# Kernel tuning notes

Measured on AMD Instinct MI355X. Metric: run time of the kernel, lower is better.

Reference implementation:

```python
import jax, jax.numpy as jnp
import numpy as np

B, T, D, H, K, V = 2, 2048, 2048, 16, 128, 128


def _l2norm(x, eps=1e-12):
    # F.normalize(p=2, dim=-1)
    n = jnp.sqrt(jnp.sum(x * x, axis=-1, keepdims=True))
    return x / jnp.maximum(n, eps)


def setup_inputs() -> dict:
    key = jax.random.key(0)
    ks = jax.random.split(key, 7)
    s = D ** -0.5
    return {
        "x": jax.random.normal(ks[0], (B, T, D), jnp.float32),
        "Wq": jax.random.normal(ks[1], (H * K, D), jnp.float32) * s,
        "Wk": jax.random.normal(ks[2], (H * K, D), jnp.float32) * s,
        "Wv": jax.random.normal(ks[3], (H * V, D), jnp.float32) * s,
        "Wa": jax.random.normal(ks[4], (H, D), jnp.float32) * s,
        "ba": jnp.zeros((H,), jnp.float32),
        "Wb": jax.random.normal(ks[5], (H, D), jnp.float32) * s,
        "bb": jnp.zeros((H,), jnp.float32),
    }


def _forward(x, Wq, Wk, Wv, Wa, ba, Wb, bb):
    Bq, Tq, _ = x.shape
    # projections (nn.Linear: y = x @ W.T)
    q = _l2norm(jnp.einsum('btd,od->bto', x, Wq).reshape(Bq, Tq, H, K))
    k = _l2norm(jnp.einsum('btd,od->bto', x, Wk).reshape(Bq, Tq, H, K))
    v = jnp.einsum('btd,od->bto', x, Wv).reshape(Bq, Tq, H, V)
    alpha = jax.nn.sigmoid(jnp.einsum('btd,hd->bth', x, Wa) + ba)          # [B,T,H] decay in (0,1)
    beta = jax.nn.softplus(jnp.einsum('btd,hd->bth', x, Wb) + bb) * K ** (-0.5)

    # gated delta rule recurrence over time (vectorized over B,H):
    #   S_t = a_t * S_{t-1} (I - b_t k_t k_t^T) + b_t v_t k_t^T ;  o_t = S_t q_t
    def step(S, inp):
        q_t, k_t, v_t, a_t, b_t = inp  # [B,H,K],[B,H,K],[B,H,V],[B,H],[B,H]
        Sd = S * a_t[..., None, None]                              # decay  [B,H,V,K]
        pred = jnp.einsum('bhvk,bhk->bhv', Sd, k_t)                # S k
        u = b_t[..., None] * (v_t - pred)                          # delta update [B,H,V]
        S_new = Sd + u[..., None] * k_t[:, :, None, :]             # rank-1 write
        o_t = jnp.einsum('bhvk,bhk->bhv', S_new, q_t)
        return S_new, o_t

    S0 = jnp.zeros((Bq, H, V, K), x.dtype)
    xs = (q.transpose(1, 0, 2, 3), k.transpose(1, 0, 2, 3),
          v.transpose(1, 0, 2, 3), alpha.transpose(1, 0, 2), beta.transpose(1, 0, 2))
    _, o = jax.lax.scan(step, S0, xs)
    return o.transpose(1, 0, 2, 3)  # [B,T,H,V]


def reference(x, Wq, Wk, Wv, Wa, ba, Wb, bb):
    return _forward(x, Wq, Wk, Wv, Wa, ba, Wb, bb)
```

## Files before the change

kernel.cpp:

```cpp
#include <hip/hip_runtime.h>
#include <math.h>

#define BB 2
#define TT 2048
#define DD 2048
#define HH 16
#define KK 128

typedef _Float16 h4 __attribute__((ext_vector_type(4)));
typedef _Float16 v8h __attribute__((ext_vector_type(8)));
typedef float v4f __attribute__((ext_vector_type(4)));
typedef float f2 __attribute__((ext_vector_type(2)));
typedef unsigned int u2v __attribute__((ext_vector_type(2)));

__global__ __launch_bounds__(256) void gemm_nt3(const float* __restrict__ A,
                                                const float* __restrict__ W0,
                                                const float* __restrict__ W1,
                                                const float* __restrict__ W2,
                                                float* __restrict__ Cbase,
                                                int M, int N, int Kd) {
  __shared__ float As[8][128];
  __shared__ float Bs[8][128];
  const int z = blockIdx.z;
  const float* W = (z == 0) ? W0 : (z == 1) ? W1 : W2;
  float* C = Cbase + (size_t)z * M * N;
  const int tid = threadIdx.x;
  const int bm = blockIdx.y * 128;
  const int bn = blockIdx.x * 128;
  const int lrow = tid >> 1;
  const int lcol = (tid & 1) * 4;
  const int rm = (tid >> 4) * 8;
  const int rn = (tid & 15) * 8;
  const float* Ap = A + (size_t)(bm + lrow) * Kd + lcol;
  const float* Wp = W + (size_t)(bn + lrow) * Kd + lcol;
  float acc[8][8];
#pragma unroll
  for (int i = 0; i < 8; i++)
#pragma unroll
    for (int j = 0; j < 8; j++) acc[i][j] = 0.f;
  float4 av = *(const float4*)Ap;
  float4 wv = *(const float4*)Wp;
  for (int d0 = 0; d0 < Kd; d0 += 8) {
    __syncthreads();
    As[lcol + 0][lrow] = av.x; As[lcol + 1][lrow] = av.y;
    As[lcol + 2][lrow] = av.z; As[lcol + 3][lrow] = av.w;
    Bs[lcol + 0][lrow] = wv.x; Bs[lcol + 1][lrow] = wv.y;
    Bs[lcol + 2][lrow] = wv.z; Bs[lcol + 3][lrow] = wv.w;
    __syncthreads();
    if (d0 + 8 < Kd) {
      av = *(const float4*)(Ap + d0 + 8);
      wv = *(const float4*)(Wp + d0 + 8);
    }
#pragma unroll
    for (int kk = 0; kk < 8; kk++) {
      const float4 a0 = *(const float4*)&As[kk][rm];
      const float4 a1 = *(const float4*)&As[kk][rm + 4];
      const float4 b0 = *(const float4*)&Bs[kk][rn];
      const float4 b1 = *(const float4*)&Bs[kk][rn + 4];
      const float ar[8] = {a0.x, a0.y, a0.z, a0.w, a1.x, a1.y, a1.z, a1.w};
      const float br[8] = {b0.x, b0.y, b0.z, b0.w, b1.x, b1.y, b1.z, b1.w};
#pragma unroll
      for (int i = 0; i < 8; i++)
#pragma unroll
        for (int j = 0; j < 8; j++) acc[i][j] = fmaf(ar[i], br[j], acc[i][j]);
    }
  }
#pragma unroll
  for (int i = 0; i < 8; i++) {
    float* cp = C + (size_t)(bm + rm + i) * N + bn + rn;
    float4 c0 = {acc[i][0], acc[i][1], acc[i][2], acc[i][3]};
    float4 c1 = {acc[i][4], acc[i][5], acc[i][6], acc[i][7]};
    *(float4*)cp = c0;
    *(float4*)(cp + 4) = c1;
  }
}

__global__ __launch_bounds__(256) void convert_f16(
    const float* __restrict__ x, const float* __restrict__ Wq,
    const float* __restrict__ Wk, const float* __restrict__ Wv,
    _Float16* __restrict__ xh, _Float16* __restrict__ Wf) {
  const size_t N4X = (size_t)BB * TT * DD / 4;
  const size_t N4W = (size_t)(HH * KK) * DD / 4;
  const size_t i = (size_t)blockIdx.x * 256 + threadIdx.x;
  if (i < N4X) {
    const float4 v = ((const float4*)x)[i];
    h4 hi;
    hi.x = (_Float16)v.x; hi.y = (_Float16)v.y;
    hi.z = (_Float16)v.z; hi.w = (_Float16)v.w;
    ((h4*)xh)[i] = hi;
  } else {
    const size_t j = i - N4X;
    const float* Ws = (j < N4W) ? Wq : (j < 2 * N4W) ? Wk : Wv;
    const size_t jj = (j < N4W) ? j : (j < 2 * N4W) ? (j - N4W) : (j - 2 * N4W);
    const float4 v = ((const float4*)Ws)[jj];
    h4 hi;
    hi.x = (_Float16)v.x; hi.y = (_Float16)v.y;
    hi.z = (_Float16)v.z; hi.w = (_Float16)v.w;
    ((h4*)Wf)[j] = hi;
  }
}

#define GLDS(gp, lp)                                              \
  __builtin_amdgcn_global_load_lds(                               \
      (const __attribute__((address_space(1))) void*)(gp),        \
      (__attribute__((address_space(3))) void*)(lp), 16, 0, 0)

__global__ __launch_bounds__(256) void gemm_mfma(
    const _Float16* __restrict__ xh, const _Float16* __restrict__ Wf,
    float* __restrict__ Cbase) {
  __shared__ float4 lraw[1024];
  _Float16* Ah = (_Float16*)lraw;
  _Float16* Bs = Ah + 4096;

  const int z = blockIdx.z;
  const _Float16* W = Wf + (size_t)z * DD * (HH * KK);
  float* C = Cbase + (size_t)z * (BB * TT) * (HH * KK);

  const int tid = threadIdx.x;
  const int w = tid >> 6;
  const int lane = tid & 63;
  const int bm = blockIdx.y * 128;
  const int bn = blockIdx.x * 128;
  const int wm = (w & 1) * 64;
  const int wn = (w >> 1) * 64;
  const int m16 = lane & 15;
  const int quad = lane >> 4;

  const _Float16* gA = xh + (size_t)(bm + (tid >> 2)) * DD + (tid & 3) * 8;
  const _Float16* gB = W + (size_t)(bn + (tid >> 2)) * DD + (tid & 3) * 8;
  const int lb = w * 512;

  v4f acc[4][4];
#pragma unroll
  for (int i = 0; i < 4; i++)
#pragma unroll
    for (int j = 0; j < 4; j++) acc[i][j] = (v4f){0.f, 0.f, 0.f, 0.f};

  for (int d0 = 0; d0 < DD; d0 += 32) {
    GLDS(gA + d0, Ah + lb);
    GLDS(gA + d0 + 64 * DD, Ah + 2048 + lb);
    GLDS(gB + d0, Bs + lb);
    GLDS(gB + d0 + 64 * DD, Bs + 2048 + lb);
    __syncthreads();
    v8h ah[4], bw[4];
#pragma unroll
    for (int i = 0; i < 4; i++) {
      ah[i] = *(const v8h*)&Ah[(wm + i * 16 + m16) * 32 + quad * 8];
      bw[i] = *(const v8h*)&Bs[(wn + i * 16 + m16) * 32 + quad * 8];
    }
#pragma unroll
    for (int mi = 0; mi < 4; mi++)
#pragma unroll
      for (int ni = 0; ni < 4; ni++)
        acc[mi][ni] = __builtin_amdgcn_mfma_f32_16x16x32_f16(ah[mi], bw[ni],
                                                             acc[mi][ni], 0, 0, 0);
    __syncthreads();
  }
#pragma unroll
  for (int mi = 0; mi < 4; mi++) {
#pragma unroll
    for (int r = 0; r < 4; r++) {
      float* cp =
          C + (size_t)(bm + wm + mi * 16 + quad * 4 + r) * (HH * KK) + bn + wn + m16;
#pragma unroll
      for (int ni = 0; ni < 4; ni++) cp[ni * 16] = acc[mi][ni][r];
    }
  }
}

__global__ __launch_bounds__(64) void ab_proj(const float* __restrict__ x,
                                              const float* __restrict__ Wa,
                                              const float* __restrict__ ba,
                                              const float* __restrict__ Wb,
                                              const float* __restrict__ bb,
                                              float* __restrict__ abq) {
  const int row = blockIdx.x;
  const int g = blockIdx.y;
  const int h0 = (g & 1) * 8;
  const bool isA = (g < 2);
  const float* W = isA ? Wa : Wb;
  const int lane = threadIdx.x;
  const float* xr = x + (size_t)row * DD;
  float acc[8];
#pragma unroll
  for (int j = 0; j < 8; j++) acc[j] = 0.f;
  for (int d = lane; d < DD; d += 64) {
    const float xv = xr[d];
#pragma unroll
    for (int j = 0; j < 8; j++)
      acc[j] = fmaf(xv, W[(size_t)(h0 + j) * DD + d], acc[j]);
  }
#pragma unroll
  for (int j = 0; j < 8; j++) {
#pragma unroll
    for (int off = 32; off > 0; off >>= 1) acc[j] += __shfl_xor(acc[j], off, 64);
  }
  if (lane == 0) {
    if (isA) {
#pragma unroll
      for (int j = 0; j < 8; j++) {
        const float z = acc[j] + ba[h0 + j];
        abq[((size_t)row * HH + h0 + j) * 4 + 0] = 1.0f / (1.0f + expf(-z));
      }
    } else {
#pragma unroll
      for (int j = 0; j < 8; j++) {
        const float z = acc[j] + bb[h0 + j];
        const float sp = (z > 20.f) ? z : log1pf(expf(z));
        abq[((size_t)row * HH + h0 + j) * 4 + 1] = sp * 0.08838834764831845f;
      }
    }
  }
}

__global__ __launch_bounds__(256) void norm_qk(float* __restrict__ q,
                                               float* __restrict__ k,
                                               float* __restrict__ abq) {
  const int vec = blockIdx.x * 4 + (threadIdx.x >> 6);
  const int l = threadIdx.x & 63;
  float* qp = q + (size_t)vec * 128;
  float* kp = k + (size_t)vec * 128;
  float q0 = qp[l], q1 = qp[l + 64];
  float k0 = kp[l], k1 = kp[l + 64];
  float sq = q0 * q0 + q1 * q1;
  float sk = k0 * k0 + k1 * k1;
#pragma unroll
  for (int off = 32; off > 0; off >>= 1) {
    sq += __shfl_xor(sq, off, 64);
    sk += __shfl_xor(sk, off, 64);
  }
  const float iq = 1.0f / fmaxf(sqrtf(sq), 1e-12f);
  const float ik = 1.0f / fmaxf(sqrtf(sk), 1e-12f);
  q0 *= iq; q1 *= iq; k0 *= ik; k1 *= ik;
  qp[l] = q0; qp[l + 64] = q1;
  kp[l] = k0; kp[l + 64] = k1;
  float pq = q0 * k0 + q1 * k1;
#pragma unroll
  for (int off = 32; off > 0; off >>= 1) pq += __shfl_xor(pq, off, 64);
  if (l == 0) abq[(size_t)vec * 4 + 2] = pq;
}

#define DPP_ADD(x, ctrl)                                                     \
  ((x) + __int_as_float(__builtin_amdgcn_update_dpp(                         \
             0, __float_as_int(x), (ctrl), 0xF, 0xF, true)))

__device__ __forceinline__ float xadd32(float x) {
  const u2v r = __builtin_amdgcn_permlane32_swap(__float_as_uint(x),
                                                 __float_as_uint(x), false,
                                                 false);
  return __uint_as_float(r.x) + __uint_as_float(r.y);
}

#define SCAN_STEP(kc, qc, vc, ac, jj)                                          \
  {                                                                            \
    const f2 ka = {kc.x, kc.y};                                                \
    const f2 kb2 = {kc.z, kc.w};                                               \
    const f2 qa = {qc.x, qc.y};                                                \
    const f2 qb2 = {qc.z, qc.w};                                               \
    const f2 pdk = __builtin_elementwise_fma(Sb, kb2, Sa * ka);                \
    const f2 pdq = __builtin_elementwise_fma(Sb, qb2, Sa * qa);                \
    float dk = pdk.x + pdk.y;                                                  \
    float dq = pdq.x + pdq.y;                                                  \
    dk = DPP_ADD(dk, 0xB1);  dq = DPP_ADD(dq, 0xB1);             \
    dk = DPP_ADD(dk, 0x4E);  dq = DPP_ADD(dq, 0x4E);             \
    dk = DPP_ADD(dk, 0x141); dq = DPP_ADD(dq, 0x141);            \
    dk = DPP_ADD(dk, 0x140); dq = DPP_ADD(dq, 0x140);            \
    dk = xadd32(dk);         dq = xadd32(dq);                    \
    const float u = ac.y * fmaf(-ac.x, dk, vc);                                \
    const float oo = fmaf(ac.x, dq, u * ac.z);                                 \
    const f2 a2 = {ac.x, ac.x};                                                \
    const f2 u2 = {u, u};                                                      \
    Sa = __builtin_elementwise_fma(a2, Sa, u2 * ka);                           \
    Sb = __builtin_elementwise_fma(a2, Sb, u2 * kb2);                          \
    obuf = (ks == (jj)) ? oo : obuf;                                           \
  }

#define PD 8

__global__ __launch_bounds__(256, 2) void scan_kernel(
    const float* __restrict__ q, const float* __restrict__ k,
    const float* __restrict__ v, const float* __restrict__ abq,
    float* __restrict__ o) {
  const int bid = blockIdx.x;
  const int bh = bid & 31;
  const int s = bid >> 5;
  const int h = bh & 15;
  const int b = bh >> 4;
  const int tid = threadIdx.x;
  const int w = tid >> 6;
  const int lane = tid & 63;
  const int rg = (lane >> 4) & 1;
  const int ks = (lane & 15) | ((lane >> 5) << 4);
  const int vrow = s * 8 + w * 2 + rg;

  const size_t base = (size_t)b * TT * 2048 + (size_t)h * KK;
  const float* kU = k + base;
  const float* qU = q + base;
  const float* vU = v + base;
  const float* aU = abq + ((size_t)b * TT * HH + h) * 4;
  float* oU = o + base;
  const int vks = ks * 4;

  f2 Sa = {0.f, 0.f}, Sb = {0.f, 0.f};
  float obuf = 0.f;

  float4 kf[PD], qf[PD], af[PD];
  float vf[PD];
#pragma unroll
  for (int d = 0; d < PD; d++) {
    kf[d] = *(const float4*)(kU + vks + d * 2048);
    qf[d] = *(const float4*)(qU + vks + d * 2048);
    vf[d] = vU[vrow + d * 2048];
    af[d] = *(const float4*)(aU + d * 64);
  }

  int off = 0;
  int aoff = 0;
  for (int t0 = 0; t0 < TT - PD; t0 += PD) {
#pragma unroll
    for (int j = 0; j < PD; j++) {
      SCAN_STEP(kf[j], qf[j], vf[j], af[j], j);
      kf[j] = *(const float4*)(kU + vks + off + (j + PD) * 2048);
      qf[j] = *(const float4*)(qU + vks + off + (j + PD) * 2048);
      vf[j] = vU[vrow + off + (j + PD) * 2048];
      af[j] = *(const float4*)(aU + aoff + (j + PD) * 64);
      __builtin_amdgcn_sched_barrier(0);
    }
    if (ks < 8) oU[vrow + off + ks * 2048] = obuf;
    off += PD * 2048;
    aoff += PD * 64;
  }
#pragma unroll
  for (int j = 0; j < PD; j++) {
    SCAN_STEP(kf[j], qf[j], vf[j], af[j], j);
  }
  if (ks < 8) oU[vrow + off + ks * 2048] = obuf;
}

extern "C" void kernel_launch(void* const* d_in, const int* in_sizes, int n_in,
                              void* d_out, int out_size, void* d_ws,
                              size_t ws_size, hipStream_t stream) {
  const float* x = (const float*)d_in[0];
  const float* Wq = (const float*)d_in[1];
  const float* Wk = (const float*)d_in[2];
  const float* Wv = (const float*)d_in[3];
  const float* Wa = (const float*)d_in[4];
  const float* ba = (const float*)d_in[5];
  const float* Wb = (const float*)d_in[6];
  const float* bb = (const float*)d_in[7];
  float* out = (float*)d_out;
  float* ws = (float*)d_ws;

  const size_t PROJ = (size_t)BB * TT * HH * KK;
  const size_t NABQ = (size_t)BB * TT * HH * 4;
  float* qw = ws;
  float* kw = ws + PROJ;
  float* vw = ws + 2 * PROJ;
  float* abq = ws + 3 * PROJ;
  _Float16* xh = (_Float16*)(abq + NABQ);
  _Float16* Wf = xh + (size_t)BB * TT * DD;
  const size_t NEED = (3 * PROJ + NABQ) * 4 +
                      ((size_t)BB * TT * DD + 3 * (size_t)(HH * KK) * DD) * 2;

  const int M = BB * TT;
  const int N = HH * KK;
  if (ws_size >= NEED) {
    const int cgrid = (int)(((size_t)BB * TT * DD / 4 + 3 * (size_t)N * DD / 4) / 256);
    convert_f16<<<cgrid, 256, 0, stream>>>(x, Wq, Wk, Wv, xh, Wf);
    gemm_mfma<<<dim3(N / 128, M / 128, 3), 256, 0, stream>>>(xh, Wf, qw);
  } else {
    gemm_nt3<<<dim3(N / 128, M / 128, 3), 256, 0, stream>>>(x, Wq, Wk, Wv, qw,
                                                            M, N, DD);
  }
  ab_proj<<<dim3(M, 4), 64, 0, stream>>>(x, Wa, ba, Wb, bb, abq);
  norm_qk<<<(BB * TT * HH) / 4, 256, 0, stream>>>(qw, kw, abq);
  scan_kernel<<<BB * HH * 16, 256, 0, stream>>>(qw, kw, vw, abq, out);
}
```

Baseline: 726.0 us.

## Double-buffer k/q/gate tiles in LDS via direct global-to-LDS loads in scan

The recurrent scan kernel no longer loads k, q and gate vectors into per-thread register prefetch arrays. Instead, each workgroup stages groups of 8 timesteps into double-buffered shared memory using direct global-to-LDS loads, with explicit vmcnt waits and workgroup barriers, and reads them back from LDS during compute. The goal is to cut redundant global traffic and register pressure from the per-lane prefetch pipeline. The cost is two block-wide barriers per 8-step group on a latency-bound serial recurrence, plus extra LDS reads on the critical path.

```diff
diff --git a/kernel.cpp b/kernel.cpp
--- a/kernel.cpp
+++ b/kernel.cpp
@@ -251,7 +251,10 @@
   return __uint_as_float(r.x) + __uint_as_float(r.y);
 }
 
-#define SCAN_STEP(kc, qc, vc, ac, jj)                                          \
+#define SBAR() asm volatile("s_barrier" ::: "memory")
+#define WAITV(n) asm volatile("s_waitcnt vmcnt(" #n ")" ::: "memory")
+
+#define SCAN_MATH(kc, qc, vc, ac, jj, obname)                                  \
   {                                                                            \
     const f2 ka = {kc.x, kc.y};                                                \
     const f2 kb2 = {kc.z, kc.w};                                               \
@@ -272,15 +275,40 @@
     const f2 u2 = {u, u};                                                      \
     Sa = __builtin_elementwise_fma(a2, Sa, u2 * ka);                           \
     Sb = __builtin_elementwise_fma(a2, Sb, u2 * kb2);                          \
-    obuf = (ks == (jj)) ? oo : obuf;                                           \
-  }
-
-#define PD 8
+    obname = (ks == (jj)) ? oo : obname;                                       \
+  }
+
+#define STAGE(bi, tg)                                                          \
+  {                                                                            \
+    const float* gk =                                                          \
+        kU + (size_t)((tg) + 2 * w + (lane >> 5)) * 2048 + (lane & 31) * 4;    \
+    GLDS(gk, &Kb[bi][2 * w][0]);                                               \
+    const float* gq =                                                          \
+        qU + (size_t)((tg) + 2 * w + (lane >> 5)) * 2048 + (lane & 31) * 4;    \
+    GLDS(gq, &Qb[bi][2 * w][0]);                                               \
+    if (lane < 8) GLDS(aU + (size_t)((tg) + lane) * 64, &Ab[bi][0][0]);        \
+    _Pragma("unroll") for (int jj = 0; jj < 8; jj++)                           \
+        vf##bi[jj] = vU[vrow + (size_t)((tg) + jj) * 2048];                    \
+  }
+
+#define COMPUTE_GROUP(bi, obname)                                              \
+  float obname = 0.f;                                                          \
+  _Pragma("unroll") for (int j = 0; j < 8; j++) {                              \
+    const float4 kc = *(const float4*)&Kb[bi][j][ks4];                         \
+    const float4 qc = *(const float4*)&Qb[bi][j][ks4];                         \
+    const float4 ac = *(const float4*)&Ab[bi][j][0];                           \
+    const float vc = vf##bi[j];                                                \
+    SCAN_MATH(kc, qc, vc, ac, j, obname);                                      \
+  }
 
 __global__ __launch_bounds__(256, 2) void scan_kernel(
     const float* __restrict__ q, const float* __restrict__ k,
     const float* __restrict__ v, const float* __restrict__ abq,
     float* __restrict__ o) {
+  __shared__ float Kb[2][8][128];
+  __shared__ float Qb[2][8][128];
+  __shared__ float Ab[2][8][4];
+
   const int bid = blockIdx.x;
   const int bh = bid & 31;
   const int s = bid >> 5;
@@ -291,6 +319,7 @@
   const int lane = tid & 63;
   const int rg = (lane >> 4) & 1;
   const int ks = (lane & 15) | ((lane >> 5) << 4);
+  const int ks4 = ks * 4;
   const int vrow = s * 8 + w * 2 + rg;
 
   const size_t base = (size_t)b * TT * 2048 + (size_t)h * KK;
@@ -299,42 +328,44 @@
   const float* vU = v + base;
   const float* aU = abq + ((size_t)b * TT * HH + h) * 4;
   float* oU = o + base;
-  const int vks = ks * 4;
 
   f2 Sa = {0.f, 0.f}, Sb = {0.f, 0.f};
-  float obuf = 0.f;
-
-  float4 kf[PD], qf[PD], af[PD];
-  float vf[PD];
-#pragma unroll
-  for (int d = 0; d < PD; d++) {
-    kf[d] = *(const float4*)(kU + vks + d * 2048);
-    qf[d] = *(const float4*)(qU + vks + d * 2048);
-    vf[d] = vU[vrow + d * 2048];
-    af[d] = *(const float4*)(aU + d * 64);
-  }
-
-  int off = 0;
-  int aoff = 0;
-  for (int t0 = 0; t0 < TT - PD; t0 += PD) {
-#pragma unroll
-    for (int j = 0; j < PD; j++) {
-      SCAN_STEP(kf[j], qf[j], vf[j], af[j], j);
-      kf[j] = *(const float4*)(kU + vks + off + (j + PD) * 2048);
-      qf[j] = *(const float4*)(qU + vks + off + (j + PD) * 2048);
-      vf[j] = vU[vrow + off + (j + PD) * 2048];
-      af[j] = *(const float4*)(aU + aoff + (j + PD) * 64);
-      __builtin_amdgcn_sched_barrier(0);
-    }
-    if (ks < 8) oU[vrow + off + ks * 2048] = obuf;
-    off += PD * 2048;
-    aoff += PD * 64;
-  }
-#pragma unroll
-  for (int j = 0; j < PD; j++) {
-    SCAN_STEP(kf[j], qf[j], vf[j], af[j], j);
-  }
-  if (ks < 8) oU[vrow + off + ks * 2048] = obuf;
+  float vf0[8], vf1[8];
+
+  STAGE(0, 0);
+  STAGE(1, 8);
+  WAITV(11);
+  SBAR();
+  __builtin_amdgcn_sched_barrier(0);
+
+  int tg = 0;
+  for (int gp = 0; gp < TT / 8; gp += 2) {
+    COMPUTE_GROUP(0, ob0);
+    if (ks < 8) oU[vrow + (size_t)(tg + ks) * 2048] = ob0;
+    SBAR();
+    if (gp + 2 < TT / 8) {
+      STAGE(0, tg + 16);
+      WAITV(11);
+    } else {
+      WAITV(0);
+    }
+    SBAR();
+    __builtin_amdgcn_sched_barrier(0);
+
+    COMPUTE_GROUP(1, ob1);
+    if (ks < 8) oU[vrow + (size_t)(tg + 8 + ks) * 2048] = ob1;
+    SBAR();
+    if (gp + 3 < TT / 8) {
+      STAGE(1, tg + 24);
+      WAITV(11);
+    } else {
+      WAITV(0);
+    }
+    SBAR();
+    __builtin_amdgcn_sched_barrier(0);
+
+    tg += 16;
+  }
 }
 
 extern "C" void kernel_launch(void* const* d_in, const int* in_sizes, int n_in,
```

Measured after the change: 720.6 us. Within noise of the previous version (-0.7%).
